# Performance work log

Measured on AMD Instinct MI355X. Metric: run time of the kernel, lower is better.

## Reference

```python
import jax, jax.numpy as jnp
import numpy as np

VOCAB = 100000
D = 128
B = 256
L = 2048  # leaves per tree (power of two -> complete binary tree)


def setup_inputs() -> dict:
    key = jax.random.key(0)
    k1, k2, k3, k4 = jax.random.split(key, 4)
    word_ids = jax.random.randint(k1, (B, L), 0, VOCAB)
    embedding = jax.random.normal(k2, (VOCAB, D), dtype=jnp.float32) * 0.1
    # torch nn.Linear(2*D, D): weight [D, 2*D], bias [D]
    W = jax.random.normal(k3, (D, 2 * D), dtype=jnp.float32) * (1.0 / np.sqrt(2 * D))
    b = jax.random.normal(k4, (D,), dtype=jnp.float32) * 0.01
    return {"word_ids": word_ids, "embedding": embedding, "W": W, "b": b}


def reference(word_ids, embedding, W, b):
    # Leaves: embedding lookup for every leaf of every tree. [B, L, D]
    x = embedding[word_ids]
    # Internal nodes, batched by depth: each level combines adjacent pairs
    # via linear(concat(left, right)). log2(L) levels (static unroll).
    while x.shape[1] > 1:
        left = x[:, 0::2, :]   # [B, n/2, D]
        right = x[:, 1::2, :]  # [B, n/2, D]
        pair = jnp.concatenate([left, right], axis=-1)  # [B, n/2, 2D]
        x = jnp.einsum('bnd,od->bno', pair, W) + b      # [B, n/2, D]
    return x[:, 0, :]  # root result per tree, [B, D]
```

## Files before the change

### kernel.cpp

```cpp
#include <hip/hip_runtime.h>


typedef __bf16 bf16x8 __attribute__((ext_vector_type(8)));
typedef __bf16 bf16x4 __attribute__((ext_vector_type(4)));
typedef float f32x4 __attribute__((ext_vector_type(4)));

__device__ __forceinline__ int sw_off(int row, int col) {
    return row * 128 + ((((col >> 3) ^ (row & 15)) << 3) | (col & 7));
}

__global__ void pack_w_kernel(const float* __restrict__ W,
                              __bf16* __restrict__ wpack) {
    const int gf = blockIdx.x;
    const int l = threadIdx.x;
    const int nt = gf >> 3, kk = gf & 7;
    const int o = nt * 16 + (l & 15);
    const int d = kk * 32 + ((l >> 4) << 3);
    const float* src = W + o * 256 + d;
    bf16x8 h;
#pragma unroll
    for (int j = 0; j < 8; ++j) h[j] = (__bf16)src[j];
    *(bf16x8*)(wpack + (size_t)(gf * 64 + l) * 8) = h;
}

template <int NOUT>
__device__ __forceinline__ void step_tile(
    const __bf16* __restrict__ src, __bf16* __restrict__ dst,
    const bf16x8* wf, const float* bval, int nw, int q, int lm)
{
    const int me = (NOUT >= 16) ? lm : (lm < NOUT ? lm : 0);
    f32x4 acc[4];
#pragma unroll
    for (int nl = 0; nl < 4; ++nl)
        acc[nl] = (f32x4){ bval[nl], bval[nl], bval[nl], bval[nl] };
#pragma unroll
    for (int kk = 0; kk < 8; ++kk) {
        const int row = 2 * me + (kk >> 2);
        const int col = (kk & 3) * 32 + q * 8;
        const bf16x8 af = *(const bf16x8*)&src[sw_off(row, col)];
#pragma unroll
        for (int nl = 0; nl < 4; ++nl)
            acc[nl] = __builtin_amdgcn_mfma_f32_16x16x32_bf16(
                af, wf[nl * 8 + kk], acc[nl], 0, 0, 0);
    }
#pragma unroll
    for (int nl = 0; nl < 4; ++nl) {
        const int col = (nw * 4 + nl) * 16 + lm;
        const bf16x4 hv = __builtin_convertvector(acc[nl], bf16x4);
#pragma unroll
        for (int r = 0; r < 4; ++r) {
            const int row = q * 4 + r;
            if (NOUT >= 16 || row < NOUT)
                dst[sw_off(row, col)] = hv[r];
        }
    }
}

__device__ __forceinline__ void final_tile(
    const __bf16* __restrict__ src, __bf16* __restrict__ yrow,
    const bf16x8* wf, const float* bval, int nw, int q, int lm)
{
    const int me = (lm < 2) ? lm : 0;
    f32x4 acc[4];
#pragma unroll
    for (int nl = 0; nl < 4; ++nl)
        acc[nl] = (f32x4){ bval[nl], bval[nl], bval[nl], bval[nl] };
#pragma unroll
    for (int kk = 0; kk < 8; ++kk) {
        const int row = 2 * me + (kk >> 2);
        const int col = (kk & 3) * 32 + q * 8;
        const bf16x8 af = *(const bf16x8*)&src[sw_off(row, col)];
#pragma unroll
        for (int nl = 0; nl < 4; ++nl)
            acc[nl] = __builtin_amdgcn_mfma_f32_16x16x32_bf16(
                af, wf[nl * 8 + kk], acc[nl], 0, 0, 0);
    }
#pragma unroll
    for (int nl = 0; nl < 4; ++nl) {
        const int col = (nw * 4 + nl) * 16 + lm;
        if (q == 0) {
            yrow[0 * 128 + col] = (__bf16)acc[nl][0];
            yrow[1 * 128 + col] = (__bf16)acc[nl][1];
        }
    }
}

__global__ __launch_bounds__(256, 2) void tree128_kernel(
    const int* __restrict__ wid, const float* __restrict__ emb,
    const __bf16* __restrict__ wpack, const float* __restrict__ bias,
    __bf16* __restrict__ yout)
{
    __shared__ __align__(16) __bf16 A[128 * 128];
    __shared__ __align__(16) __bf16 S[32 * 128];
    const int tid = threadIdx.x;
    const int batch = blockIdx.x >> 4;
    const int grp = blockIdx.x & 15;
    const int wv = tid >> 6, nw = wv & 1, mw = wv >> 1;
    const int ln = tid & 63, q = ln >> 4, lm = ln & 15;

    {
        const int* wb = wid + batch * 2048 + grp * 128;
        int idreg[16];
#pragma unroll
        for (int i = 0; i < 16; ++i) idreg[i] = wb[(tid >> 5) + 8 * i];
#pragma unroll
        for (int i = 0; i < 16; ++i) {
            const int row = (tid >> 5) + 8 * i;
            const int c4 = tid & 31;
            const f32x4 v =
                *(const f32x4*)(emb + (size_t)idreg[i] * 128 + c4 * 4);
            *(bf16x4*)&A[sw_off(row, c4 * 4)] =
                __builtin_convertvector(v, bf16x4);
        }
    }

    bf16x8 wf[32];
    const bf16x8* wp = (const bf16x8*)wpack;
#pragma unroll
    for (int f = 0; f < 32; ++f) wf[f] = wp[(nw * 32 + f) * 64 + ln];
    float bval[4];
#pragma unroll
    for (int nl = 0; nl < 4; ++nl) bval[nl] = bias[(nw * 4 + nl) * 16 + lm];

    __syncthreads();

    step_tile<16>(A + mw * 32 * 128, S + mw * 16 * 128, wf, bval, nw, q, lm);
    __syncthreads();
    step_tile<16>(A + (64 + mw * 32) * 128, A + mw * 16 * 128,
                  wf, bval, nw, q, lm);
    __syncthreads();
    step_tile<16>(mw ? A : S, A + (32 + mw * 16) * 128, wf, bval, nw, q, lm);
    __syncthreads();
    if (mw == 0) step_tile<16>(A + 32 * 128, S, wf, bval, nw, q, lm);
    __syncthreads();
    if (mw == 0) step_tile<8>(S, A, wf, bval, nw, q, lm);
    __syncthreads();
    if (mw == 0) step_tile<4>(A, S, wf, bval, nw, q, lm);
    __syncthreads();
    if (mw == 0)
        final_tile(S, yout + (size_t)(batch * 32 + grp * 2) * 128,
                   wf, bval, nw, q, lm);
}

#define STRIDE 136
__global__ __launch_bounds__(256) void tree32_kernel(
    const __bf16* __restrict__ yin, const __bf16* __restrict__ wpack,
    const float* __restrict__ bias, float* __restrict__ out)
{
    __shared__ __align__(16) __bf16 buf[2][32 * STRIDE];
    const int tid = threadIdx.x;
    const int batch = blockIdx.x;
    const int wv = tid >> 6, ln = tid & 63, q = ln >> 4, lm = ln & 15;

    bf16x8 wf[16];
    const bf16x8* wp = (const bf16x8*)wpack;
#pragma unroll
    for (int f = 0; f < 16; ++f) wf[f] = wp[(16 * wv + f) * 64 + ln];
    float bval[2];
    bval[0] = bias[(2 * wv + 0) * 16 + lm];
    bval[1] = bias[(2 * wv + 1) * 16 + lm];

#pragma unroll
    for (int i = 0; i < 2; ++i) {
        const int flat = tid + 256 * i;
        const int row = flat >> 4;
        const int c8 = flat & 15;
        const bf16x8 v =
            *(const bf16x8*)(yin + (size_t)(batch * 32 + row) * 128 + c8 * 8);
        *(bf16x8*)&buf[0][row * STRIDE + c8 * 8] = v;
    }
    __syncthreads();

    int nin = 32, rb = 0;
    while (nin > 1) {
        const int nout = nin >> 1;
        const int me = (lm < nout) ? lm : 0;
        bf16x8 af[8];
#pragma unroll
        for (int kk = 0; kk < 8; ++kk) {
            const int hi = kk >> 2;
            const int col = (kk & 3) * 32 + q * 8;
            af[kk] = *(const bf16x8*)&buf[rb][(2 * me + hi) * STRIDE + col];
        }
#pragma unroll
        for (int nl = 0; nl < 2; ++nl) {
            f32x4 acc = { bval[nl], bval[nl], bval[nl], bval[nl] };
#pragma unroll
            for (int kk = 0; kk < 8; ++kk)
                acc = __builtin_amdgcn_mfma_f32_16x16x32_bf16(
                    af[kk], wf[nl * 8 + kk], acc, 0, 0, 0);
            const int col = (2 * wv + nl) * 16 + lm;
            if (nout == 1) {
                if (q == 0) out[(size_t)batch * 128 + col] = acc[0];
            } else {
                const bf16x4 hv = __builtin_convertvector(acc, bf16x4);
#pragma unroll
                for (int r = 0; r < 4; ++r) {
                    const int row = q * 4 + r;
                    if (row < nout)
                        buf[rb ^ 1][row * STRIDE + col] = hv[r];
                }
            }
        }
        __syncthreads();
        rb ^= 1;
        nin = nout;
    }
}

extern "C" void kernel_launch(void* const* d_in, const int* in_sizes, int n_in,
                              void* d_out, int out_size, void* d_ws, size_t ws_size,
                              hipStream_t stream) {
    const int*   wid = (const int*)d_in[0];
    const float* emb = (const float*)d_in[1];
    const float* W   = (const float*)d_in[2];
    const float* b   = (const float*)d_in[3];
    float* out = (float*)d_out;

    __bf16* wpack = (__bf16*)d_ws;
    __bf16* y     = wpack + 32768;

    pack_w_kernel<<<64, 64, 0, stream>>>(W, wpack);
    tree128_kernel<<<4096, 256, 0, stream>>>(wid, emb, wpack, b, y);
    tree32_kernel<<<256, 256, 0, stream>>>(y, wpack, b, out);
}
```

Before: 145.5 us.

## Split tree work across waves by output columns and stop level-one tree at eight nodes

The leaf kernel now gives each of its four waves two 16-column output tiles with 16 weight fragments, instead of splitting rows and columns across wave pairs with 32 fragments. It stops after four levels and emits eight nodes per 128-leaf group rather than two, which leaves more levels to the second kernel. The second kernel now reduces 128 nodes per tree using the same step routine in one swizzled shared buffer. Fewer registers per wave and no idle waves in the later levels should raise occupancy. In exchange it writes four times more intermediate data to global memory and puts more serial levels in the low-parallelism 256-block finish kernel.

```diff
diff --git a/kernel.cpp b/kernel.cpp
--- a/kernel.cpp
+++ b/kernel.cpp
@@ -4,6 +4,8 @@
 typedef __bf16 bf16x8 __attribute__((ext_vector_type(8)));
 typedef __bf16 bf16x4 __attribute__((ext_vector_type(4)));
 typedef float f32x4 __attribute__((ext_vector_type(4)));
+
+#define NROWS 144
 
 __device__ __forceinline__ int sw_off(int row, int col) {
     return row * 128 + ((((col >> 3) ^ (row & 15)) << 3) | (col & 7));
@@ -23,80 +25,75 @@
     *(bf16x8*)(wpack + (size_t)(gf * 64 + l) * 8) = h;
 }
 
-template <int NOUT>
-__device__ __forceinline__ void step_tile(
-    const __bf16* __restrict__ src, __bf16* __restrict__ dst,
-    const bf16x8* wf, const float* bval, int nw, int q, int lm)
+template <int NOUT, int MODE>
+__device__ __forceinline__ void step(
+    __bf16* __restrict__ L, int off, int dstb,
+    const bf16x8* wf, const float* bval, int wv, int q, int lm)
 {
     const int me = (NOUT >= 16) ? lm : (lm < NOUT ? lm : 0);
-    f32x4 acc[4];
-#pragma unroll
-    for (int nl = 0; nl < 4; ++nl)
-        acc[nl] = (f32x4){ bval[nl], bval[nl], bval[nl], bval[nl] };
+    f32x4 acc[2];
+    acc[0] = (f32x4){ bval[0], bval[0], bval[0], bval[0] };
+    acc[1] = (f32x4){ bval[1], bval[1], bval[1], bval[1] };
 #pragma unroll
     for (int kk = 0; kk < 8; ++kk) {
-        const int row = 2 * me + (kk >> 2);
+        const int j = 2 * me + (kk >> 2);
+        const int row = MODE ? (j < 16 ? 128 + j : j - 16) : off + j;
         const int col = (kk & 3) * 32 + q * 8;
-        const bf16x8 af = *(const bf16x8*)&src[sw_off(row, col)];
-#pragma unroll
-        for (int nl = 0; nl < 4; ++nl)
-            acc[nl] = __builtin_amdgcn_mfma_f32_16x16x32_bf16(
-                af, wf[nl * 8 + kk], acc[nl], 0, 0, 0);
-    }
-#pragma unroll
-    for (int nl = 0; nl < 4; ++nl) {
-        const int col = (nw * 4 + nl) * 16 + lm;
+        const bf16x8 af = *(const bf16x8*)&L[sw_off(row, col)];
+        acc[0] = __builtin_amdgcn_mfma_f32_16x16x32_bf16(af, wf[kk],     acc[0], 0, 0, 0);
+        acc[1] = __builtin_amdgcn_mfma_f32_16x16x32_bf16(af, wf[8 + kk], acc[1], 0, 0, 0);
+    }
+#pragma unroll
+    for (int nl = 0; nl < 2; ++nl) {
+        const int col = (2 * wv + nl) * 16 + lm;
         const bf16x4 hv = __builtin_convertvector(acc[nl], bf16x4);
 #pragma unroll
         for (int r = 0; r < 4; ++r) {
             const int row = q * 4 + r;
             if (NOUT >= 16 || row < NOUT)
-                dst[sw_off(row, col)] = hv[r];
-        }
-    }
-}
-
-__device__ __forceinline__ void final_tile(
-    const __bf16* __restrict__ src, __bf16* __restrict__ yrow,
-    const bf16x8* wf, const float* bval, int nw, int q, int lm)
-{
-    const int me = (lm < 2) ? lm : 0;
-    f32x4 acc[4];
-#pragma unroll
-    for (int nl = 0; nl < 4; ++nl)
-        acc[nl] = (f32x4){ bval[nl], bval[nl], bval[nl], bval[nl] };
+                L[sw_off(dstb + row, col)] = hv[r];
+        }
+    }
+}
+
+__device__ __forceinline__ void step8_to_global(
+    const __bf16* __restrict__ L, int off, __bf16* __restrict__ yrow,
+    const bf16x8* wf, const float* bval, int wv, int q, int lm)
+{
+    const int me = (lm < 8) ? lm : 0;
+    f32x4 acc[2];
+    acc[0] = (f32x4){ bval[0], bval[0], bval[0], bval[0] };
+    acc[1] = (f32x4){ bval[1], bval[1], bval[1], bval[1] };
 #pragma unroll
     for (int kk = 0; kk < 8; ++kk) {
-        const int row = 2 * me + (kk >> 2);
+        const int j = 2 * me + (kk >> 2);
         const int col = (kk & 3) * 32 + q * 8;
-        const bf16x8 af = *(const bf16x8*)&src[sw_off(row, col)];
-#pragma unroll
-        for (int nl = 0; nl < 4; ++nl)
-            acc[nl] = __builtin_amdgcn_mfma_f32_16x16x32_bf16(
-                af, wf[nl * 8 + kk], acc[nl], 0, 0, 0);
-    }
-#pragma unroll
-    for (int nl = 0; nl < 4; ++nl) {
-        const int col = (nw * 4 + nl) * 16 + lm;
-        if (q == 0) {
-            yrow[0 * 128 + col] = (__bf16)acc[nl][0];
-            yrow[1 * 128 + col] = (__bf16)acc[nl][1];
-        }
-    }
-}
-
-__global__ __launch_bounds__(256, 2) void tree128_kernel(
+        const bf16x8 af = *(const bf16x8*)&L[sw_off(off + j, col)];
+        acc[0] = __builtin_amdgcn_mfma_f32_16x16x32_bf16(af, wf[kk],     acc[0], 0, 0, 0);
+        acc[1] = __builtin_amdgcn_mfma_f32_16x16x32_bf16(af, wf[8 + kk], acc[1], 0, 0, 0);
+    }
+#pragma unroll
+    for (int nl = 0; nl < 2; ++nl) {
+        const int col = (2 * wv + nl) * 16 + lm;
+#pragma unroll
+        for (int r = 0; r < 4; ++r) {
+            const int row = q * 4 + r;
+            if (row < 8)
+                yrow[(size_t)row * 128 + col] = (__bf16)acc[nl][r];
+        }
+    }
+}
+
+__global__ __launch_bounds__(256) void tree128_kernel(
     const int* __restrict__ wid, const float* __restrict__ emb,
     const __bf16* __restrict__ wpack, const float* __restrict__ bias,
     __bf16* __restrict__ yout)
 {
-    __shared__ __align__(16) __bf16 A[128 * 128];
-    __shared__ __align__(16) __bf16 S[32 * 128];
+    __shared__ __align__(16) __bf16 L[NROWS * 128];
     const int tid = threadIdx.x;
     const int batch = blockIdx.x >> 4;
     const int grp = blockIdx.x & 15;
-    const int wv = tid >> 6, nw = wv & 1, mw = wv >> 1;
-    const int ln = tid & 63, q = ln >> 4, lm = ln & 15;
+    const int wv = tid >> 6, ln = tid & 63, q = ln >> 4, lm = ln & 15;
 
     {
         const int* wb = wid + batch * 2048 + grp * 128;
@@ -109,48 +106,10 @@
             const int c4 = tid & 31;
             const f32x4 v =
                 *(const f32x4*)(emb + (size_t)idreg[i] * 128 + c4 * 4);
-            *(bf16x4*)&A[sw_off(row, c4 * 4)] =
+            *(bf16x4*)&L[sw_off(row, c4 * 4)] =
                 __builtin_convertvector(v, bf16x4);
         }
     }
-
-    bf16x8 wf[32];
-    const bf16x8* wp = (const bf16x8*)wpack;
-#pragma unroll
-    for (int f = 0; f < 32; ++f) wf[f] = wp[(nw * 32 + f) * 64 + ln];
-    float bval[4];
-#pragma unroll
-    for (int nl = 0; nl < 4; ++nl) bval[nl] = bias[(nw * 4 + nl) * 16 + lm];
-
-    __syncthreads();
-
-    step_tile<16>(A + mw * 32 * 128, S + mw * 16 * 128, wf, bval, nw, q, lm);
-    __syncthreads();
-    step_tile<16>(A + (64 + mw * 32) * 128, A + mw * 16 * 128,
-                  wf, bval, nw, q, lm);
-    __syncthreads();
-    step_tile<16>(mw ? A : S, A + (32 + mw * 16) * 128, wf, bval, nw, q, lm);
-    __syncthreads();
-    if (mw == 0) step_tile<16>(A + 32 * 128, S, wf, bval, nw, q, lm);
-    __syncthreads();
-    if (mw == 0) step_tile<8>(S, A, wf, bval, nw, q, lm);
-    __syncthreads();
-    if (mw == 0) step_tile<4>(A, S, wf, bval, nw, q, lm);
-    __syncthreads();
-    if (mw == 0)
-        final_tile(S, yout + (size_t)(batch * 32 + grp * 2) * 128,
-                   wf, bval, nw, q, lm);
-}
-
-#define STRIDE 136
-__global__ __launch_bounds__(256) void tree32_kernel(
-    const __bf16* __restrict__ yin, const __bf16* __restrict__ wpack,
-    const float* __restrict__ bias, float* __restrict__ out)
-{
-    __shared__ __align__(16) __bf16 buf[2][32 * STRIDE];
-    const int tid = threadIdx.x;
-    const int batch = blockIdx.x;
-    const int wv = tid >> 6, ln = tid & 63, q = ln >> 4, lm = ln & 15;
 
     bf16x8 wf[16];
     const bf16x8* wp = (const bf16x8*)wpack;
@@ -160,51 +119,87 @@
     bval[0] = bias[(2 * wv + 0) * 16 + lm];
     bval[1] = bias[(2 * wv + 1) * 16 + lm];
 
-#pragma unroll
-    for (int i = 0; i < 2; ++i) {
+    __syncthreads();
+    step<16, 0>(L, 0, 128, wf, bval, wv, q, lm);
+    __syncthreads();
+    step<16, 0>(L, 32, 0, wf, bval, wv, q, lm);
+    __syncthreads();
+    step<16, 0>(L, 64, 16, wf, bval, wv, q, lm);
+    step<16, 0>(L, 96, 32, wf, bval, wv, q, lm);
+    __syncthreads();
+    step<16, 1>(L, 0, 48, wf, bval, wv, q, lm);
+    step<16, 0>(L, 16, 64, wf, bval, wv, q, lm);
+    __syncthreads();
+    step<16, 0>(L, 48, 0, wf, bval, wv, q, lm);
+    __syncthreads();
+    step8_to_global(L, 0, yout + (size_t)(batch * 128 + grp * 8) * 128,
+                    wf, bval, wv, q, lm);
+}
+
+__global__ __launch_bounds__(256) void finish_kernel(
+    const __bf16* __restrict__ yin, const __bf16* __restrict__ wpack,
+    const float* __restrict__ bias, float* __restrict__ out)
+{
+    __shared__ __align__(16) __bf16 L[NROWS * 128];
+    const int tid = threadIdx.x;
+    const int batch = blockIdx.x;
+    const int wv = tid >> 6, ln = tid & 63, q = ln >> 4, lm = ln & 15;
+
+    bf16x8 wf[16];
+    const bf16x8* wp = (const bf16x8*)wpack;
+#pragma unroll
+    for (int f = 0; f < 16; ++f) wf[f] = wp[(16 * wv + f) * 64 + ln];
+    float bval[2];
+    bval[0] = bias[(2 * wv + 0) * 16 + lm];
+    bval[1] = bias[(2 * wv + 1) * 16 + lm];
+
+#pragma unroll
+    for (int i = 0; i < 8; ++i) {
         const int flat = tid + 256 * i;
         const int row = flat >> 4;
         const int c8 = flat & 15;
         const bf16x8 v =
-            *(const bf16x8*)(yin + (size_t)(batch * 32 + row) * 128 + c8 * 8);
-        *(bf16x8*)&buf[0][row * STRIDE + c8 * 8] = v;
-    }
-    __syncthreads();
-
-    int nin = 32, rb = 0;
-    while (nin > 1) {
-        const int nout = nin >> 1;
-        const int me = (lm < nout) ? lm : 0;
-        bf16x8 af[8];
+            *(const bf16x8*)(yin + (size_t)(batch * 128 + row) * 128 + c8 * 8);
+        *(bf16x8*)&L[sw_off(row, c8 * 8)] = v;
+    }
+    __syncthreads();
+
+    step<16, 0>(L, 0, 128, wf, bval, wv, q, lm);
+    __syncthreads();
+    step<16, 0>(L, 32, 0, wf, bval, wv, q, lm);
+    __syncthreads();
+    step<16, 0>(L, 64, 16, wf, bval, wv, q, lm);
+    step<16, 0>(L, 96, 32, wf, bval, wv, q, lm);
+    __syncthreads();
+    step<16, 1>(L, 0, 48, wf, bval, wv, q, lm);
+    step<16, 0>(L, 16, 64, wf, bval, wv, q, lm);
+    __syncthreads();
+    step<16, 0>(L, 48, 0, wf, bval, wv, q, lm);
+    __syncthreads();
+    step<8, 0>(L, 0, 16, wf, bval, wv, q, lm);
+    __syncthreads();
+    step<4, 0>(L, 16, 0, wf, bval, wv, q, lm);
+    __syncthreads();
+    step<2, 0>(L, 0, 8, wf, bval, wv, q, lm);
+    __syncthreads();
+
+    {
+        f32x4 acc[2];
+        acc[0] = (f32x4){ bval[0], bval[0], bval[0], bval[0] };
+        acc[1] = (f32x4){ bval[1], bval[1], bval[1], bval[1] };
 #pragma unroll
         for (int kk = 0; kk < 8; ++kk) {
-            const int hi = kk >> 2;
+            const int row = 8 + (kk >> 2);
             const int col = (kk & 3) * 32 + q * 8;
-            af[kk] = *(const bf16x8*)&buf[rb][(2 * me + hi) * STRIDE + col];
-        }
-#pragma unroll
-        for (int nl = 0; nl < 2; ++nl) {
-            f32x4 acc = { bval[nl], bval[nl], bval[nl], bval[nl] };
-#pragma unroll
-            for (int kk = 0; kk < 8; ++kk)
-                acc = __builtin_amdgcn_mfma_f32_16x16x32_bf16(
-                    af[kk], wf[nl * 8 + kk], acc, 0, 0, 0);
-            const int col = (2 * wv + nl) * 16 + lm;
-            if (nout == 1) {
-                if (q == 0) out[(size_t)batch * 128 + col] = acc[0];
-            } else {
-                const bf16x4 hv = __builtin_convertvector(acc, bf16x4);
-#pragma unroll
-                for (int r = 0; r < 4; ++r) {
-                    const int row = q * 4 + r;
-                    if (row < nout)
-                        buf[rb ^ 1][row * STRIDE + col] = hv[r];
-                }
-            }
-        }
-        __syncthreads();
-        rb ^= 1;
-        nin = nout;
+            const bf16x8 af = *(const bf16x8*)&L[sw_off(row, col)];
+            acc[0] = __builtin_amdgcn_mfma_f32_16x16x32_bf16(af, wf[kk],     acc[0], 0, 0, 0);
+            acc[1] = __builtin_amdgcn_mfma_f32_16x16x32_bf16(af, wf[8 + kk], acc[1], 0, 0, 0);
+        }
+        if (q == 0) {
+#pragma unroll
+            for (int nl = 0; nl < 2; ++nl)
+                out[(size_t)batch * 128 + (2 * wv + nl) * 16 + lm] = acc[nl][0];
+        }
     }
 }
 
@@ -222,5 +217,5 @@
 
     pack_w_kernel<<<64, 64, 0, stream>>>(W, wpack);
     tree128_kernel<<<4096, 256, 0, stream>>>(wid, emb, wpack, b, y);
-    tree32_kernel<<<256, 256, 0, stream>>>(y, wpack, b, out);
-}
+    finish_kernel<<<256, 256, 0, stream>>>(y, wpack, b, out);
+}
```

After: 149.1 us. 2.5% more time.
